# Performance work log

Hardware: AMD Instinct MI355X
Metric: run time of the kernel (lower is better)

## Reference

```python
import jax, jax.numpy as jnp
import numpy as np

B, D, N, P, MAXG, K = 1024, 128, 131072, 64, 2048, 16


def _l2norm(x, eps=1e-12):
    # matches torch F.normalize: x / clamp_min(||x||, eps)
    return x / jnp.maximum(jnp.linalg.norm(x, axis=-1, keepdims=True), eps)


def setup_inputs() -> dict:
    key = jax.random.key(0)
    ks = jax.random.split(key, 7)
    query = jax.random.normal(ks[0], (B, D), jnp.float32)
    keys = jax.random.normal(ks[1], (N, D), jnp.float32)
    vals = jax.random.normal(ks[2], (N, D), jnp.float32)
    labels = jax.random.normal(ks[3], (N,), jnp.float32)
    hard_assignment = jax.random.randint(ks[4], (B,), 0, P)
    cached_groups = jax.random.randint(ks[5], (P, MAXG), 0, N)
    group_sizes = jax.random.randint(ks[6], (P,), K, MAXG + 1)
    # -1 padding beyond each group's size, as in cache_sample_groups
    pos = jnp.arange(MAXG)[None, :]
    cached_groups = jnp.where(pos < group_sizes[:, None], cached_groups, -1)
    return dict(query=query, keys=keys, vals=vals, labels=labels,
                hard_assignment=hard_assignment, cached_groups=cached_groups,
                group_sizes=group_sizes, k=K)


def reference(query, keys, vals, labels, hard_assignment, cached_groups, group_sizes, k):
    n = keys.shape[0]
    q_norm = _l2norm(query)                                  # (B, D)
    grp = group_sizes[hard_assignment]                       # (B,)
    normal = grp >= k                                        # fallback mask (grp<k -> zeros)
    cand = cached_groups[hard_assignment]                    # (B, G) padded with -1
    valid = cand >= 0
    safe = jnp.clip(cand, 0, n - 1)
    keys_c = _l2norm(keys[safe])                             # (B, G, D) gathered + normalized
    sim = jnp.einsum('bd,bgd->bg', q_norm, keys_c)           # cosine similarity
    sim = jnp.where(valid, sim, -1e9)                        # mask padded candidates
    _, top = jax.lax.top_k(sim, k)                           # (B, k) positions within group
    i_final = jnp.take_along_axis(safe, top, axis=1)         # (B, k) memory-bank indices
    nk = keys[i_final]                                       # (B, k, D)
    nv = vals[i_final]                                       # (B, k, D)
    nl = labels[jnp.clip(i_final, 0, n - 1)]                 # (B, k)
    m = normal[:, None]
    nk = jnp.where(m[..., None], nk, 0.0)
    nv = jnp.where(m[..., None], nv, 0.0)
    nl = jnp.where(m, nl, 0.0)
    top_k_idx = jnp.where(m, i_final, 0)
    return nk, nv, nl, top_k_idx
```

## Files before the change

### kernel.cpp

```cpp
#include <hip/hip_runtime.h>

#define DIMS 128
#define KTOP 16
#define SMAX 2048
#define SLICE 64
#define CK 64
#define QT 14
#define CQ 14
#define NTHR 128

__device__ __forceinline__ unsigned long long packsim(float v, int g) {
    unsigned u = __float_as_uint(v);
    u = (u & 0x80000000u) ? ~u : (u | 0x80000000u);
    return ((unsigned long long)u << 32) | (unsigned)(0xFFFFFFFFu - (unsigned)g);
}

__global__ __launch_bounds__(1024)
void bucket_kernel(const int* __restrict__ hard_assign,
                   int* __restrict__ qcount, int* __restrict__ qlist, int B, int P)
{
    const int t = threadIdx.x;
    for (int i = t; i < P; i += 1024) qcount[i] = 0;
    __syncthreads();
    for (int b = t; b < B; b += 1024) {
        const int p = hard_assign[b];
        const int slot = atomicAdd(&qcount[p], 1);
        qlist[(size_t)p * B + slot] = b;
    }
}

__global__ __launch_bounds__(NTHR)
void score_kernel(const float* __restrict__ query,
                  const float* __restrict__ keys,
                  const int*   __restrict__ cached_groups,
                  const int*   __restrict__ qcount,
                  const int*   __restrict__ qlist,
                  float* __restrict__ sims,
                  int B, int N, int MAXG, int nslice)
{
    __shared__ float s_keyT[DIMS * CK];
    __shared__ float s_qT[DIMS * CQ];
    __shared__ float s_inv[SLICE];
    __shared__ int   s_g[SLICE];
    __shared__ int   s_qb[QT];

    const int p = blockIdx.x / nslice;
    const int s = blockIdx.x % nslice;
    const int cnt = qcount[p];
    if (cnt == 0) return;

    const int t = threadIdx.x;
    const int base = s * SLICE;
    const int* gp = cached_groups + (size_t)p * MAXG;
    const int* ql = qlist + (size_t)p * B;

    {
        const int r    = t >> 1;
        const int half = t & 1;
        const int cand = (base + r < MAXG) ? gp[base + r] : -1;
        if (half == 0) s_g[r] = cand;
        const int sf = cand < 0 ? 0 : (cand > N - 1 ? N - 1 : cand);
        const float* kr = keys + (size_t)sf * DIMS + half * 64;
        float ks = 0.0f;
        #pragma unroll
        for (int h = 0; h < 2; ++h) {
            float4 v[8];
            #pragma unroll
            for (int i = 0; i < 8; ++i)
                v[i] = *(const float4*)(kr + h * 32 + i * 4);
            #pragma unroll
            for (int i = 0; i < 8; ++i) {
                const int d = half * 64 + h * 32 + i * 4;
                ks += v[i].x * v[i].x + v[i].y * v[i].y
                    + v[i].z * v[i].z + v[i].w * v[i].w;
                s_keyT[(d + 0) * CK + r] = v[i].x;
                s_keyT[(d + 1) * CK + r] = v[i].y;
                s_keyT[(d + 2) * CK + r] = v[i].z;
                s_keyT[(d + 3) * CK + r] = v[i].w;
            }
        }
        ks += __shfl_xor(ks, 1, 64);
        if (half == 0) s_inv[r] = 1.0f / fmaxf(sqrtf(ks), 1e-12f);
    }

    const int qg = t >> 4;
    const int q0 = qg * 2;
    const int qr0 = (qg < 7) ? q0 : 0;
    const int c0 = (t & 15) * 4;

    for (int qbase = 0; qbase < cnt; qbase += QT) {
        {
            const int q    = t & 15;
            const int dblk = t >> 4;
            if (q < QT) {
                const int ii = qbase + q;
                const int sq = ql[(ii < cnt) ? ii : (cnt - 1)];
                if (dblk == 0) s_qb[q] = sq;
                const float* qr = query + (size_t)sq * DIMS + dblk * 16;
                #pragma unroll
                for (int i = 0; i < 4; ++i) {
                    const float4 v = *(const float4*)(qr + i * 4);
                    const int d = dblk * 16 + i * 4;
                    s_qT[(d + 0) * CQ + q] = v.x;
                    s_qT[(d + 1) * CQ + q] = v.y;
                    s_qT[(d + 2) * CQ + q] = v.z;
                    s_qT[(d + 3) * CQ + q] = v.w;
                }
            }
        }
        __syncthreads();

        float acc[2][4];
        #pragma unroll
        for (int a = 0; a < 2; ++a)
            #pragma unroll
            for (int bb = 0; bb < 4; ++bb) acc[a][bb] = 0.0f;

        #pragma unroll 8
        for (int k = 0; k < DIMS; ++k) {
            const float2 aq = *(const float2*)&s_qT[k * CQ + qr0];
            const float4 bk = *(const float4*)&s_keyT[k * CK + c0];
            acc[0][0] += aq.x * bk.x; acc[0][1] += aq.x * bk.y;
            acc[0][2] += aq.x * bk.z; acc[0][3] += aq.x * bk.w;
            acc[1][0] += aq.y * bk.x; acc[1][1] += aq.y * bk.y;
            acc[1][2] += aq.y * bk.z; acc[1][3] += aq.y * bk.w;
        }

        const float4 inv = *(const float4*)&s_inv[c0];
        const int4   gv  = *(const int4*)&s_g[c0];
        #pragma unroll
        for (int qi = 0; qi < 2; ++qi) {
            const int ii = qbase + q0 + qi;
            if (qg < 7 && ii < cnt) {
                const int b = s_qb[q0 + qi];
                float4 o;
                o.x = (gv.x >= 0) ? acc[qi][0] * inv.x : -1.0e9f;
                o.y = (gv.y >= 0) ? acc[qi][1] * inv.y : -1.0e9f;
                o.z = (gv.z >= 0) ? acc[qi][2] * inv.z : -1.0e9f;
                o.w = (gv.w >= 0) ? acc[qi][3] * inv.w : -1.0e9f;
                float* dst = sims + (size_t)b * MAXG + base + c0;
                if (base + c0 + 3 < MAXG) {
                    *(float4*)dst = o;
                } else {
                    if (base + c0 + 0 < MAXG) dst[0] = o.x;
                    if (base + c0 + 1 < MAXG) dst[1] = o.y;
                    if (base + c0 + 2 < MAXG) dst[2] = o.z;
                }
            }
        }

        if (qbase + QT < cnt) __syncthreads();
    }
}

#define CASW(x,y) { if ((x) < (y)) { const unsigned long long _t = (x); (x) = (y); (y) = _t; } }

__global__ __launch_bounds__(256)
void topk_gather_kernel(const float* __restrict__ keys,
                        const float* __restrict__ vals,
                        const float* __restrict__ labels,
                        const int*   __restrict__ hard_assign,
                        const int*   __restrict__ cached_groups,
                        const int*   __restrict__ group_sizes,
                        const float* __restrict__ sims,
                        float* __restrict__ out,
                        int B, int MAXG)
{
    const int b = blockIdx.x, t = threadIdx.x;
    const int lane = t & 63, w = t >> 6;
    const int sub = t & 15, cg = t >> 4;

    __shared__ unsigned long long s_merge[64];
    __shared__ int s_wing[KTOP];

    const int p = hard_assign[b];
    const int grpsz = group_sizes[p];
    const bool normal = (grpsz >= KTOP);
    const int* gptr = cached_groups + (size_t)p * MAXG;
    const float* simrow = sims + (size_t)b * MAXG;

    unsigned long long k0, k1, k2, k3, k4, k5, k6, k7;
    {
        #define LDK(j) ({ const int g = w * (SMAX / 4) + (j) * 64 + lane;          \
                          const float v = (g < MAXG) ? simrow[g] : -3.0e38f;       \
                          packsim(v, g); })
        k0 = LDK(0); k1 = LDK(1); k2 = LDK(2); k3 = LDK(3);
        k4 = LDK(4); k5 = LDK(5); k6 = LDK(6); k7 = LDK(7);
        #undef LDK
    }
    CASW(k0,k1) CASW(k2,k3) CASW(k4,k5) CASW(k6,k7)
    CASW(k0,k2) CASW(k1,k3) CASW(k4,k6) CASW(k5,k7)
    CASW(k1,k2) CASW(k5,k6)
    CASW(k0,k4) CASW(k1,k5) CASW(k2,k6) CASW(k3,k7)
    CASW(k2,k4) CASW(k3,k5)
    CASW(k1,k2) CASW(k3,k4) CASW(k5,k6)

    #pragma unroll 1
    for (int r = 0; r < KTOP; ++r) {
        unsigned long long wm = k0;
        #pragma unroll
        for (int off = 1; off < 64; off <<= 1) {
            const unsigned long long o = __shfl_xor(wm, off, 64);
            wm = (o > wm) ? o : wm;
        }
        if (lane == 0) s_merge[w * KTOP + r] = wm;
        if (k0 == wm) {
            k0 = k1; k1 = k2; k2 = k3; k3 = k4;
            k4 = k5; k5 = k6; k6 = k7; k7 = 0ull;
        }
    }
    __syncthreads();

    if (w == 0) {
        unsigned long long u = s_merge[lane];
        #pragma unroll
        for (int k = 2; k <= 64; k <<= 1) {
            #pragma unroll
            for (int j = k >> 1; j > 0; j >>= 1) {
                const unsigned long long o = __shfl_xor(u, j, 64);
                const bool low = (lane & j) == 0;
                const bool asc = (lane & k) == 0;
                const unsigned long long mn = (u < o) ? u : o;
                const unsigned long long mx = (u < o) ? o : u;
                u = (low == asc) ? mn : mx;
            }
        }
        if (lane >= 64 - KTOP)
            s_wing[63 - lane] = (int)(0xFFFFFFFFu - (unsigned)(u & 0xFFFFFFFFull));
    }
    __syncthreads();

    const int g    = s_wing[cg];
    const int cand = gptr[g];
    const int idx  = cand < 0 ? 0 : cand;

    const size_t BK = (size_t)B * KTOP;
    float* out_nk = out;
    float* out_nv = out + BK * DIMS;
    float* out_nl = out + 2 * BK * DIMS;
    float* out_id = out_nl + BK;

    const size_t od = ((size_t)b * KTOP + cg) * DIMS + sub * 8;
    if (normal) {
        const float* kr = keys + (size_t)idx * DIMS + sub * 8;
        const float* vr = vals + (size_t)idx * DIMS + sub * 8;
        *(float4*)(out_nk + od)     = *(const float4*)(kr);
        *(float4*)(out_nk + od + 4) = *(const float4*)(kr + 4);
        *(float4*)(out_nv + od)     = *(const float4*)(vr);
        *(float4*)(out_nv + od + 4) = *(const float4*)(vr + 4);
        if (sub == 0) {
            out_nl[(size_t)b * KTOP + cg] = labels[idx];
            out_id[(size_t)b * KTOP + cg] = (float)idx;
        }
    } else {
        const float4 z = make_float4(0.f, 0.f, 0.f, 0.f);
        *(float4*)(out_nk + od)     = z;
        *(float4*)(out_nk + od + 4) = z;
        *(float4*)(out_nv + od)     = z;
        *(float4*)(out_nv + od + 4) = z;
        if (sub == 0) {
            out_nl[(size_t)b * KTOP + cg] = 0.0f;
            out_id[(size_t)b * KTOP + cg] = 0.0f;
        }
    }
}

extern "C" void kernel_launch(void* const* d_in, const int* in_sizes, int n_in,
                              void* d_out, int out_size, void* d_ws, size_t ws_size,
                              hipStream_t stream) {
    const float* query  = (const float*)d_in[0];
    const float* keys   = (const float*)d_in[1];
    const float* vals   = (const float*)d_in[2];
    const float* labels = (const float*)d_in[3];
    const int* hard_assign   = (const int*)d_in[4];
    const int* cached_groups = (const int*)d_in[5];
    const int* group_sizes   = (const int*)d_in[6];

    const int B = in_sizes[0] / DIMS;
    const int N = in_sizes[1] / DIMS;
    const int P = in_sizes[6];
    const int MAXG = in_sizes[5] / P;
    const int nslice = (MAXG + SLICE - 1) / SLICE;

    float* sims  = (float*)d_ws;
    int* qcount  = (int*)((char*)d_ws + (size_t)B * MAXG * 4);
    int* qlist   = qcount + P;

    bucket_kernel<<<1, 1024, 0, stream>>>(hard_assign, qcount, qlist, B, P);

    score_kernel<<<P * nslice, NTHR, 0, stream>>>(
        query, keys, cached_groups, qcount, qlist, sims, B, N, MAXG, nslice);

    topk_gather_kernel<<<B, 256, 0, stream>>>(
        keys, vals, labels, hard_assign, cached_groups, group_sizes, sims,
        (float*)d_out, B, MAXG);
}
```

Measured before the change: 55.70 us.

## Double block to 256 threads and overlap first query load with key staging

The similarity kernel block grows to 256 threads and each query tile grows from 14 to 32 queries, so each staged key slice is reused across more queries with fewer loop iterations. Half the threads stage and normalize keys while the other half load the first query tile at the same time, which removes one barrier from the prologue. Idle lanes from the old 14-query mapping go away. The cost is more shared memory and threads per block, which may lower occupancy, and the launch configuration must be updated to match NTHR.

Measured after the change: 51.18 us. 8.1% less time.

```diff
diff --git a/kernel.cpp b/kernel.cpp
--- a/kernel.cpp
+++ b/kernel.cpp
@@ -5,9 +5,9 @@
 #define SMAX 2048
 #define SLICE 64
 #define CK 64
-#define QT 14
-#define CQ 14
-#define NTHR 128
+#define QT 32
+#define CQ 32
+#define NTHR 256
 
 __device__ __forceinline__ unsigned long long packsim(float v, int g) {
     unsigned u = __float_as_uint(v);
@@ -54,7 +54,7 @@
     const int* gp = cached_groups + (size_t)p * MAXG;
     const int* ql = qlist + (size_t)p * B;
 
-    {
+    if (t < 128) {
         const int r    = t >> 1;
         const int half = t & 1;
         const int cand = (base + r < MAXG) ? gp[base + r] : -1;
@@ -81,35 +81,29 @@
         }
         ks += __shfl_xor(ks, 1, 64);
         if (half == 0) s_inv[r] = 1.0f / fmaxf(sqrtf(ks), 1e-12f);
-    }
-
-    const int qg = t >> 4;
-    const int q0 = qg * 2;
-    const int qr0 = (qg < 7) ? q0 : 0;
+    } else {
+        const int tq   = t - 128;
+        const int q    = tq & 31;
+        const int dblk = tq >> 5;
+        const int sq   = ql[(q < cnt) ? q : (cnt - 1)];
+        if (dblk == 0) s_qb[q] = sq;
+        const float* qr = query + (size_t)sq * DIMS + dblk * 32;
+        #pragma unroll
+        for (int i = 0; i < 8; ++i) {
+            const float4 v = *(const float4*)(qr + i * 4);
+            const int d = dblk * 32 + i * 4;
+            s_qT[(d + 0) * CQ + q] = v.x;
+            s_qT[(d + 1) * CQ + q] = v.y;
+            s_qT[(d + 2) * CQ + q] = v.z;
+            s_qT[(d + 3) * CQ + q] = v.w;
+        }
+    }
+    __syncthreads();
+
+    const int q0 = (t >> 4) * 2;
     const int c0 = (t & 15) * 4;
 
-    for (int qbase = 0; qbase < cnt; qbase += QT) {
-        {
-            const int q    = t & 15;
-            const int dblk = t >> 4;
-            if (q < QT) {
-                const int ii = qbase + q;
-                const int sq = ql[(ii < cnt) ? ii : (cnt - 1)];
-                if (dblk == 0) s_qb[q] = sq;
-                const float* qr = query + (size_t)sq * DIMS + dblk * 16;
-                #pragma unroll
-                for (int i = 0; i < 4; ++i) {
-                    const float4 v = *(const float4*)(qr + i * 4);
-                    const int d = dblk * 16 + i * 4;
-                    s_qT[(d + 0) * CQ + q] = v.x;
-                    s_qT[(d + 1) * CQ + q] = v.y;
-                    s_qT[(d + 2) * CQ + q] = v.z;
-                    s_qT[(d + 3) * CQ + q] = v.w;
-                }
-            }
-        }
-        __syncthreads();
-
+    for (int qbase = 0; ; ) {
         float acc[2][4];
         #pragma unroll
         for (int a = 0; a < 2; ++a)
@@ -118,7 +112,7 @@
 
         #pragma unroll 8
         for (int k = 0; k < DIMS; ++k) {
-            const float2 aq = *(const float2*)&s_qT[k * CQ + qr0];
+            const float2 aq = *(const float2*)&s_qT[k * CQ + q0];
             const float4 bk = *(const float4*)&s_keyT[k * CK + c0];
             acc[0][0] += aq.x * bk.x; acc[0][1] += aq.x * bk.y;
             acc[0][2] += aq.x * bk.z; acc[0][3] += aq.x * bk.w;
@@ -131,7 +125,7 @@
         #pragma unroll
         for (int qi = 0; qi < 2; ++qi) {
             const int ii = qbase + q0 + qi;
-            if (qg < 7 && ii < cnt) {
+            if (ii < cnt) {
                 const int b = s_qb[q0 + qi];
                 float4 o;
                 o.x = (gv.x >= 0) ? acc[qi][0] * inv.x : -1.0e9f;
@@ -149,7 +143,29 @@
             }
         }
 
-        if (qbase + QT < cnt) __syncthreads();
+        qbase += QT;
+        if (qbase >= cnt) break;
+
+        __syncthreads();
+        if (t >= 128) {
+            const int tq   = t - 128;
+            const int q    = tq & 31;
+            const int dblk = tq >> 5;
+            const int ii   = qbase + q;
+            const int sq   = ql[(ii < cnt) ? ii : (cnt - 1)];
+            if (dblk == 0) s_qb[q] = sq;
+            const float* qr = query + (size_t)sq * DIMS + dblk * 32;
+            #pragma unroll
+            for (int i = 0; i < 8; ++i) {
+                const float4 v = *(const float4*)(qr + i * 4);
+                const int d = dblk * 32 + i * 4;
+                s_qT[(d + 0) * CQ + q] = v.x;
+                s_qT[(d + 1) * CQ + q] = v.y;
+                s_qT[(d + 2) * CQ + q] = v.z;
+                s_qT[(d + 3) * CQ + q] = v.w;
+            }
+        }
+        __syncthreads();
     }
 }
 
```
